# Kernel tuning notes

Hardware: AMD Instinct MI355X
Metric: run time of the kernel (lower is better)

The kernel has to match this reference:

```python
import jax, jax.numpy as jnp
import numpy as np

N_NODES = 50000
N_EDGES = 800000
HIDDEN = 64
HEADS = 8
ADIM = 8
CLAMP = 5.0


def _sqrt_relu(x):
    # sqrt(relu(x)) with backward-safe formulation (identical forward values)
    pos = x > 0
    return jnp.where(pos, jnp.sqrt(jnp.where(pos, x, 1.0)), 0.0)


def _scatter_softmax(score, dst, num_nodes):
    # pyg_softmax: group-wise stable softmax over edges grouped by dst
    m = jax.ops.segment_max(score, dst, num_segments=num_nodes)
    e = jnp.exp(score - m[dst])
    s = jax.ops.segment_sum(e, dst, num_segments=num_nodes)
    return e / (s[dst] + 1e-16)


def setup_inputs() -> dict:
    key = jax.random.key(0)
    ks = jax.random.split(key, 8)
    hd = HEADS * ADIM
    x = jax.random.normal(ks[0], (N_NODES, HIDDEN), dtype=jnp.float32)
    conn_feat = jax.random.normal(ks[1], (N_EDGES, HIDDEN), dtype=jnp.float32)
    edge_index = jax.random.randint(ks[2], (2, N_EDGES), 0, N_NODES)
    qkv_weight = jax.random.normal(ks[3], (3 * hd, HIDDEN), dtype=jnp.float32) * 0.1
    qkv_bias = jnp.zeros((3 * hd,), dtype=jnp.float32)
    E_weight = jax.random.normal(ks[4], (2 * hd, HIDDEN), dtype=jnp.float32) * 0.1
    E_bias = jnp.zeros((2 * hd,), dtype=jnp.float32)
    Aw = jax.random.normal(ks[5], (ADIM, HEADS, 1), dtype=jnp.float32) * 0.3
    Bw = jax.random.normal(ks[6], (ADIM, HEADS, ADIM), dtype=jnp.float32) * 0.3
    return {"x": x, "conn_feat": conn_feat, "edge_index": edge_index,
            "qkv_weight": qkv_weight, "qkv_bias": qkv_bias,
            "E_weight": E_weight, "E_bias": E_bias, "Aw": Aw, "Bw": Bw}


def reference(x, conn_feat, edge_index, qkv_weight, qkv_bias, E_weight, E_bias, Aw, Bw):
    N = x.shape[0]
    hd = HEADS * ADIM
    # packed QKV projection
    qkv = x @ qkv_weight.T + qkv_bias            # [N, 3*hd]
    Qh, Kh, Vh = jnp.split(qkv, 3, axis=-1)      # each [N, hd]
    # edge feature projection -> Ew, Eb
    Eh = (conn_feat @ E_weight.T + E_bias).reshape(-1, 2, hd)
    Ew, Eb = Eh[:, 0, :], Eh[:, 1, :]            # [E, hd]
    dst, src = edge_index[0], edge_index[1]
    # gather-compute: signed-sqrt fused score chain
    conn1 = (Qh[dst] + Kh[src]) * Ew             # [E, hd]
    conn2 = _sqrt_relu(conn1) - _sqrt_relu(-conn1)
    conn = jax.nn.relu(conn2 + Eb)               # act = relu; Eo output
    connh = conn.reshape(-1, HEADS, ADIM)        # [E, h, d]
    score = jnp.einsum('ehd,dhc->ehc', connh, Aw)  # [E, h, 1]
    score = jnp.clip(score, -CLAMP, CLAMP)
    score = _scatter_softmax(score, dst, N)
    # attn_drop_prob = 0 -> dropout is identity
    Vsrc = Vh[src].reshape(-1, HEADS, ADIM)
    agg = jax.ops.segment_sum(Vsrc * score, dst, num_segments=N)    # [N, h, d]
    rowV = jax.ops.segment_sum(connh * score, dst, num_segments=N)  # [N, h, d]
    rowV = jnp.einsum('nhd,dhc->nhc', rowV, Bw)
    No = (agg + rowV).reshape(N, hd)
    return No, conn
```

## Files before the change

kernel.cpp:

```cpp
#include <hip/hip_runtime.h>
#include <cstdint>
#include <cmath>

#define N_NODESC 50000
#define N_EDGESC 800000

typedef __bf16 bf16x8 __attribute__((ext_vector_type(8)));
typedef float  f32x4  __attribute__((ext_vector_type(4)));


__global__ __launch_bounds__(256) void k_zero(int* __restrict__ p, int n) {
  int i = blockIdx.x * 256 + threadIdx.x;
  if (i < n) p[i] = 0;
}

__global__ __launch_bounds__(256) void k_prep(const float* __restrict__ ew,
                                              char* __restrict__ out)
{
  int idx = blockIdx.x * 256 + threadIdx.x;
  int j = idx >> 3;
  int c = idx & 7;
  float4 a = *(const float4*)&ew[j * 64 + c * 8];
  float4 b = *(const float4*)&ew[j * 64 + c * 8 + 4];
  float f[8] = {a.x, a.y, a.z, a.w, b.x, b.y, b.z, b.w};
  bf16x8 hv, lv;
#pragma unroll
  for (int i = 0; i < 8; ++i) {
    float fv = f[i];
    __bf16 h = (__bf16)fv;
    hv[i] = h;
    lv[i] = (__bf16)(fv - (float)h);
  }
  int swz = c ^ (j & 7);
  *(bf16x8*)(out + j * 128 + swz * 16) = hv;
  *(bf16x8*)(out + 16384 + j * 128 + swz * 16) = lv;
}

__global__ __launch_bounds__(256) void k_qkv(
    const float* __restrict__ x, const float* __restrict__ w,
    const float* __restrict__ bias, float* __restrict__ qkv, int N)
{
  __shared__ float wT[32 * 193];
  __shared__ float xT[32 * 65];
  const int tid = threadIdx.x;
  const int node0 = blockIdx.x * 64;
  const int tn = tid & 15;
  const int tj = tid >> 4;

  float acc[4][12];
#pragma unroll
  for (int i = 0; i < 4; ++i)
#pragma unroll
    for (int p = 0; p < 12; ++p) acc[i][p] = 0.f;

  for (int kh = 0; kh < 2; ++kh) {
#pragma unroll
    for (int it = 0; it < 6; ++it) {
      int idx4 = tid + it * 256;
      int j = idx4 >> 3;
      int k4 = idx4 & 7;
      float4 a = *(const float4*)&w[j * 64 + kh * 32 + k4 * 4];
      wT[(k4 * 4 + 0) * 193 + j] = a.x;
      wT[(k4 * 4 + 1) * 193 + j] = a.y;
      wT[(k4 * 4 + 2) * 193 + j] = a.z;
      wT[(k4 * 4 + 3) * 193 + j] = a.w;
    }
#pragma unroll
    for (int it = 0; it < 2; ++it) {
      int idx4 = tid + it * 256;
      int n = idx4 >> 3;
      int k4 = idx4 & 7;
      int gn = node0 + n;
      float4 a = make_float4(0.f, 0.f, 0.f, 0.f);
      if (gn < N) a = *(const float4*)&x[gn * 64 + kh * 32 + k4 * 4];
      xT[(k4 * 4 + 0) * 65 + n] = a.x;
      xT[(k4 * 4 + 1) * 65 + n] = a.y;
      xT[(k4 * 4 + 2) * 65 + n] = a.z;
      xT[(k4 * 4 + 3) * 65 + n] = a.w;
    }
    __syncthreads();
#pragma unroll 8
    for (int k = 0; k < 32; ++k) {
      float xa[4], wa[12];
#pragma unroll
      for (int i = 0; i < 4; ++i) xa[i] = xT[k * 65 + tn * 4 + i];
#pragma unroll
      for (int p = 0; p < 12; ++p) wa[p] = wT[k * 193 + tj * 12 + p];
#pragma unroll
      for (int i = 0; i < 4; ++i)
#pragma unroll
        for (int p = 0; p < 12; ++p)
          acc[i][p] = fmaf(xa[i], wa[p], acc[i][p]);
    }
    __syncthreads();
  }

  float b[12];
#pragma unroll
  for (int p = 0; p < 12; ++p) b[p] = bias[tj * 12 + p];
#pragma unroll
  for (int i = 0; i < 4; ++i) {
    int gn = node0 + tn * 4 + i;
    if (gn < N) {
      float* o = &qkv[gn * 192 + tj * 12];
#pragma unroll
      for (int p = 0; p < 12; ++p) o[p] = acc[i][p] + b[p];
    }
  }
}

__global__ __launch_bounds__(256) void k_edge(
    const float* __restrict__ cf, const int* __restrict__ ei,
    const float* __restrict__ ebias, const char* __restrict__ ewb,
    const float* __restrict__ qkv, float* __restrict__ conn_out,
    int* __restrict__ counts, int E)
{
  __shared__ uint4 Bsh4[2048];
  char* Bsh = (char*)Bsh4;
  const int tid  = threadIdx.x;
  const int lane = tid & 63;
  const int lr   = lane & 15;
  const int lg   = lane >> 4;
  const int wave = tid >> 6;
  const int e0   = blockIdx.x * 128 + wave * 32;

  uint4 breg[8];
#pragma unroll
  for (int it = 0; it < 8; ++it)
    breg[it] = *(const uint4*)(ewb + tid * 16 + it * 4096);

  float af[2][2][8];
#pragma unroll
  for (int t = 0; t < 2; ++t)
#pragma unroll
    for (int s = 0; s < 2; ++s) {
      const float* p = &cf[(size_t)(e0 + t * 16 + lr) * 64 + s * 32 + lg * 8];
      float4 x0 = *(const float4*)p;
      float4 x1 = *(const float4*)(p + 4);
      af[t][s][0] = x0.x; af[t][s][1] = x0.y; af[t][s][2] = x0.z; af[t][s][3] = x0.w;
      af[t][s][4] = x1.x; af[t][s][5] = x1.y; af[t][s][6] = x1.z; af[t][s][7] = x1.w;
    }

#pragma unroll
  for (int it = 0; it < 8; ++it)
    *(uint4*)(Bsh + tid * 16 + it * 4096) = breg[it];

  bf16x8 ah[2][2], al[2][2];
#pragma unroll
  for (int t = 0; t < 2; ++t)
#pragma unroll
    for (int s = 0; s < 2; ++s)
#pragma unroll
      for (int i = 0; i < 8; ++i) {
        float fv = af[t][s][i];
        __bf16 h = (__bf16)fv;
        ah[t][s][i] = h;
        al[t][s][i] = (__bf16)(fv - (float)h);
      }

  __syncthreads();

  f32x4 acc[2][8];
#pragma unroll
  for (int t = 0; t < 2; ++t)
#pragma unroll
    for (int ct = 0; ct < 8; ++ct)
      acc[t][ct] = (f32x4){0.f, 0.f, 0.f, 0.f};

#pragma unroll
  for (int s = 0; s < 2; ++s) {
    const int swz = ((s * 4 + lg) ^ (lr & 7)) * 16;
#pragma unroll
    for (int ct = 0; ct < 8; ++ct) {
      const int j = ct * 16 + lr;
      const bf16x8 bh = *(const bf16x8*)(Bsh + j * 128 + swz);
      const bf16x8 bl = *(const bf16x8*)(Bsh + 16384 + j * 128 + swz);
#pragma unroll
      for (int t = 0; t < 2; ++t) {
        acc[t][ct] = __builtin_amdgcn_mfma_f32_16x16x32_bf16(ah[t][s], bh, acc[t][ct], 0, 0, 0);
        acc[t][ct] = __builtin_amdgcn_mfma_f32_16x16x32_bf16(al[t][s], bh, acc[t][ct], 0, 0, 0);
        acc[t][ct] = __builtin_amdgcn_mfma_f32_16x16x32_bf16(ah[t][s], bl, acc[t][ct], 0, 0, 0);
      }
    }
  }

  float be[4], bb[4];
#pragma unroll
  for (int ct = 0; ct < 4; ++ct) {
    be[ct] = ebias[ct * 16 + lr];
    bb[ct] = ebias[64 + ct * 16 + lr];
  }

#pragma unroll
  for (int t = 0; t < 2; ++t) {
#pragma unroll
    for (int r = 0; r < 4; ++r) {
      const int e   = e0 + t * 16 + lg * 4 + r;
      const int dst = ei[e];
      const int src = ei[E + e];
      const float* qrow = &qkv[(size_t)dst * 192];
      const float* krow = &qkv[(size_t)src * 192 + 64];
      float* orow = &conn_out[(size_t)e * 64];
#pragma unroll
      for (int ct = 0; ct < 4; ++ct) {
        const int j = ct * 16 + lr;
        float aE = acc[t][ct][r]     + be[ct];
        float aB = acc[t][ct + 4][r] + bb[ct];
        float sv = (qrow[j] + krow[j]) * aE;
        float rt = sqrtf(fabsf(sv));
        float c2 = (sv >= 0.f) ? rt : -rt;
        orow[j] = fmaxf(c2 + aB, 0.f);
      }
      if (lr == 0) atomicAdd(&counts[dst], 1);
    }
  }
}

__global__ void k_scan(const int* __restrict__ counts, int* __restrict__ offsets,
                       int* __restrict__ cursor, int n)
{
  __shared__ int sh[1024];
  const int tid = threadIdx.x;
  const int per = (n + 1023) >> 10;
  int start = tid * per;
  int end = start + per; if (end > n) end = n;
  int sum = 0;
  for (int i = start; i < end && start < n; ++i) sum += counts[i];
  sh[tid] = sum;
  __syncthreads();
  for (int off = 1; off < 1024; off <<= 1) {
    int t = (tid >= off) ? sh[tid - off] : 0;
    __syncthreads();
    if (tid >= off) sh[tid] += t;
    __syncthreads();
  }
  int incl = sh[tid];
  int run = incl - sum;
  for (int i = start; i < end && start < n; ++i) {
    offsets[i] = run; cursor[i] = run; run += counts[i];
  }
  if (tid == 1023) offsets[n] = incl;
}

__global__ __launch_bounds__(256) void k_scatter(const int* __restrict__ ei,
    int* __restrict__ cursor, int* __restrict__ perm, int E)
{
  int e = blockIdx.x * 256 + threadIdx.x;
  if (e < E) {
    int dst = ei[e];
    int pos = atomicAdd(&cursor[dst], 1);
    perm[pos] = e;
  }
}

__global__ __launch_bounds__(256) void k_node(
    const int* __restrict__ ei, const int* __restrict__ offsets,
    const int* __restrict__ perm, const float* __restrict__ conn,
    const float* __restrict__ qkv, const float* __restrict__ Aw,
    const float* __restrict__ Bw, float* __restrict__ No, int N, int E)
{
  const int lane = threadIdx.x & 63;
  int node = blockIdx.x * 4 + (threadIdx.x >> 6);
  node = __builtin_amdgcn_readfirstlane(node);
  if (node >= N) return;

  const float awv = Aw[(lane & 7) * 8 + (lane >> 3)];
  float bw[8];
#pragma unroll
  for (int dd = 0; dd < 8; ++dd) bw[dd] = Bw[dd * 64 + lane];

  const int beg = offsets[node];
  const int end = offsets[node + 1];
  float m = -INFINITY, l = 0.f, aV = 0.f, aC = 0.f;

  float c_nxt = 0.f, v_nxt = 0.f;
  if (beg < end) {
    int e = perm[beg];
    int src = ei[E + e];
    c_nxt = conn[(size_t)e * 64 + lane];
    v_nxt = qkv[src * 192 + 128 + lane];
  }
  for (int i = beg; i < end; ++i) {
    float c = c_nxt;
    float v = v_nxt;
    if (i + 1 < end) {
      int e2 = perm[i + 1];
      int s2 = ei[E + e2];
      c_nxt = conn[(size_t)e2 * 64 + lane];
      v_nxt = qkv[s2 * 192 + 128 + lane];
    }
    float t = c * awv;
    t += __shfl_xor(t, 1, 64);
    t += __shfl_xor(t, 2, 64);
    t += __shfl_xor(t, 4, 64);
    float s = fminf(fmaxf(t, -5.f), 5.f);
    float mn = fmaxf(m, s);
    float al = __expf(m - mn);
    float wgt = __expf(s - mn);
    l  = l * al + wgt;
    aV = fmaf(wgt, v, aV * al);
    aC = fmaf(wgt, c, aC * al);
    m = mn;
  }

  float inv = 1.f / (l + 1e-16f);
  float rowv = aC * inv;
  float acc = aV * inv;
  const int hbase = lane & 56;
#pragma unroll
  for (int dd = 0; dd < 8; ++dd) {
    float rr = __shfl(rowv, hbase + dd, 64);
    acc = fmaf(rr, bw[dd], acc);
  }
  No[node * 64 + lane] = acc;
}

extern "C" void kernel_launch(void* const* d_in, const int* in_sizes, int n_in,
                              void* d_out, int out_size, void* d_ws, size_t ws_size,
                              hipStream_t stream)
{
  const float* x  = (const float*)d_in[0];
  const float* cf = (const float*)d_in[1];
  const int*   ei = (const int*)d_in[2];
  const float* qw = (const float*)d_in[3];
  const float* qb = (const float*)d_in[4];
  const float* ew = (const float*)d_in[5];
  const float* eb = (const float*)d_in[6];
  const float* Aw = (const float*)d_in[7];
  const float* Bw = (const float*)d_in[8];

  float* No   = (float*)d_out;
  float* conn = (float*)d_out + (size_t)N_NODESC * 64;

  char* ws = (char*)d_ws;
  float* QKV   = (float*)(ws);
  int* counts  = (int*)(ws + 38400000);
  int* offsets = (int*)(ws + 38600000);
  int* cursor  = (int*)(ws + 38800004);
  char* ewb    = ws + 38800016;
  int* perm    = (int*)(ws + 39000004);

  k_zero<<<(N_NODESC + 255) / 256, 256, 0, stream>>>(counts, N_NODESC);
  k_prep<<<4, 256, 0, stream>>>(ew, ewb);
  k_qkv<<<(N_NODESC + 63) / 64, 256, 0, stream>>>(x, qw, qb, QKV, N_NODESC);
  k_edge<<<N_EDGESC / 128, 256, 0, stream>>>(cf, ei, eb, ewb, QKV, conn, counts, N_EDGESC);
  k_scan<<<1, 1024, 0, stream>>>(counts, offsets, cursor, N_NODESC);
  k_scatter<<<(N_EDGESC + 255) / 256, 256, 0, stream>>>(ei, cursor, perm, N_EDGESC);
  k_node<<<N_NODESC / 4, 256, 0, stream>>>(ei, offsets, perm, conn, QKV, Aw, Bw, No, N_NODESC, N_EDGESC);
}
```

Baseline: 765.1 us.

## Permute E_weight rows for vectorized edge epilogue, prefetch gathers, drop softmax max

The E_weight prep kernel now permutes output rows so that each lane's four MFMA output columns are contiguous feature indices. This lets the edge kernel load Q/K rows as float4, prefetch edge indices and gathers before the MFMA loop, and write conn as float4 instead of scalar stores. The node kernel also drops the running-max online softmax and uses plain exp, since scores are clamped to [-5,5]. That is mathematically safe but changes rounding slightly, and it raises register pressure in the edge kernel.

```diff
diff --git a/kernel.cpp b/kernel.cpp
--- a/kernel.cpp
+++ b/kernel.cpp
@@ -20,13 +20,15 @@
   int idx = blockIdx.x * 256 + threadIdx.x;
   int j = idx >> 3;
   int c = idx & 7;
-  float4 a = *(const float4*)&ew[j * 64 + c * 8];
-  float4 b = *(const float4*)&ew[j * 64 + c * 8 + 4];
-  float f[8] = {a.x, a.y, a.z, a.w, b.x, b.y, b.z, b.w};
+  int jl = j & 63;
+  int f = (j & 64) + (jl & 15) * 4 + (jl >> 4);
+  float4 a = *(const float4*)&ew[f * 64 + c * 8];
+  float4 b = *(const float4*)&ew[f * 64 + c * 8 + 4];
+  float fv8[8] = {a.x, a.y, a.z, a.w, b.x, b.y, b.z, b.w};
   bf16x8 hv, lv;
 #pragma unroll
   for (int i = 0; i < 8; ++i) {
-    float fv = f[i];
+    float fv = fv8[i];
     __bf16 h = (__bf16)fv;
     hv[i] = h;
     lv[i] = (__bf16)(fv - (float)h);
@@ -124,6 +126,14 @@
   const int wave = tid >> 6;
   const int e0   = blockIdx.x * 128 + wave * 32;
 
+  int dstv[8], srcv[8];
+#pragma unroll
+  for (int tr = 0; tr < 8; ++tr) {
+    const int e = e0 + (tr >> 2) * 16 + lg * 4 + (tr & 3);
+    dstv[tr] = ei[e];
+    srcv[tr] = ei[E + e];
+  }
+
   uint4 breg[8];
 #pragma unroll
   for (int it = 0; it < 8; ++it)
@@ -141,6 +151,13 @@
       af[t][s][4] = x1.x; af[t][s][5] = x1.y; af[t][s][6] = x1.z; af[t][s][7] = x1.w;
     }
 
+  float4 qv4[8], kv4[8];
+#pragma unroll
+  for (int tr = 0; tr < 8; ++tr) {
+    qv4[tr] = *(const float4*)&qkv[(size_t)dstv[tr] * 192 + lr * 4];
+    kv4[tr] = *(const float4*)&qkv[(size_t)srcv[tr] * 192 + 64 + lr * 4];
+  }
+
 #pragma unroll
   for (int it = 0; it < 8; ++it)
     *(uint4*)(Bsh + tid * 16 + it * 4096) = breg[it];
@@ -160,6 +177,15 @@
 
   __syncthreads();
 
+  float qk[8][4];
+#pragma unroll
+  for (int tr = 0; tr < 8; ++tr) {
+    qk[tr][0] = qv4[tr].x + kv4[tr].x;
+    qk[tr][1] = qv4[tr].y + kv4[tr].y;
+    qk[tr][2] = qv4[tr].z + kv4[tr].z;
+    qk[tr][3] = qv4[tr].w + kv4[tr].w;
+  }
+
   f32x4 acc[2][8];
 #pragma unroll
   for (int t = 0; t < 2; ++t)
@@ -185,34 +211,31 @@
   }
 
   float be[4], bb[4];
-#pragma unroll
-  for (int ct = 0; ct < 4; ++ct) {
-    be[ct] = ebias[ct * 16 + lr];
-    bb[ct] = ebias[64 + ct * 16 + lr];
-  }
-
-#pragma unroll
-  for (int t = 0; t < 2; ++t) {
-#pragma unroll
-    for (int r = 0; r < 4; ++r) {
-      const int e   = e0 + t * 16 + lg * 4 + r;
-      const int dst = ei[e];
-      const int src = ei[E + e];
-      const float* qrow = &qkv[(size_t)dst * 192];
-      const float* krow = &qkv[(size_t)src * 192 + 64];
-      float* orow = &conn_out[(size_t)e * 64];
-#pragma unroll
-      for (int ct = 0; ct < 4; ++ct) {
-        const int j = ct * 16 + lr;
-        float aE = acc[t][ct][r]     + be[ct];
-        float aB = acc[t][ct + 4][r] + bb[ct];
-        float sv = (qrow[j] + krow[j]) * aE;
-        float rt = sqrtf(fabsf(sv));
-        float c2 = (sv >= 0.f) ? rt : -rt;
-        orow[j] = fmaxf(c2 + aB, 0.f);
-      }
-      if (lr == 0) atomicAdd(&counts[dst], 1);
-    }
+  {
+    float4 bev = *(const float4*)&ebias[lr * 4];
+    float4 bbv = *(const float4*)&ebias[64 + lr * 4];
+    be[0] = bev.x; be[1] = bev.y; be[2] = bev.z; be[3] = bev.w;
+    bb[0] = bbv.x; bb[1] = bbv.y; bb[2] = bbv.z; bb[3] = bbv.w;
+  }
+
+#pragma unroll
+  for (int tr = 0; tr < 8; ++tr) {
+    const int t = tr >> 2;
+    const int r = tr & 3;
+    const int e = e0 + t * 16 + lg * 4 + r;
+    float ov[4];
+#pragma unroll
+    for (int ct = 0; ct < 4; ++ct) {
+      float aE = acc[t][ct][r]     + be[ct];
+      float aB = acc[t][ct + 4][r] + bb[ct];
+      float sv = qk[tr][ct] * aE;
+      float rt = sqrtf(fabsf(sv));
+      float c2 = (sv >= 0.f) ? rt : -rt;
+      ov[ct] = fmaxf(c2 + aB, 0.f);
+    }
+    float4 o = make_float4(ov[0], ov[1], ov[2], ov[3]);
+    *(float4*)&conn_out[(size_t)e * 64 + lr * 4] = o;
+    if (lr == 0) atomicAdd(&counts[dstv[tr]], 1);
   }
 }
 
@@ -271,7 +294,7 @@
 
   const int beg = offsets[node];
   const int end = offsets[node + 1];
-  float m = -INFINITY, l = 0.f, aV = 0.f, aC = 0.f;
+  float l = 0.f, aV = 0.f, aC = 0.f;
 
   float c_nxt = 0.f, v_nxt = 0.f;
   if (beg < end) {
@@ -294,13 +317,10 @@
     t += __shfl_xor(t, 2, 64);
     t += __shfl_xor(t, 4, 64);
     float s = fminf(fmaxf(t, -5.f), 5.f);
-    float mn = fmaxf(m, s);
-    float al = __expf(m - mn);
-    float wgt = __expf(s - mn);
-    l  = l * al + wgt;
-    aV = fmaf(wgt, v, aV * al);
-    aC = fmaf(wgt, c, aC * al);
-    m = mn;
+    float wgt = __expf(s);
+    l += wgt;
+    aV = fmaf(wgt, v, aV);
+    aC = fmaf(wgt, c, aC);
   }
 
   float inv = 1.f / (l + 1e-16f);
```

New measurement: 728.9 us. 1.05x faster.
